# Kernel optimization log

Measured on AMD Instinct MI355X. Metric: run time of the kernel, lower is better.

The kernel has to match this reference:

```python
import jax, jax.numpy as jnp
import numpy as np

NUM_CHUNKS = 8
N = 8192            # points per chunk
STRIDE = 6144
TOTAL = STRIDE * (NUM_CHUNKS - 1) + N  # 51200
OVERLAP_RATIO = 0.3


def setup_inputs() -> dict:
    key = jax.random.key(0)
    ks = jax.random.split(key, 14)
    # Points in a tiny box so all pairwise distances < threshold=0.1 -> full overlap masks.
    chunks = jax.random.uniform(ks[0], (NUM_CHUNKS, N, 3), dtype=jnp.float32) * 0.05
    s = 0.1  # small conv-weight scale keeps smoothed outputs within the threshold box
    return {
        "chunks": chunks,
        "bs_w1": jax.random.normal(ks[1], (32, 3, 5), jnp.float32) * s,
        "bs_b1": jax.random.normal(ks[2], (32,), jnp.float32) * s,
        "bs_w2": jax.random.normal(ks[3], (32, 32, 5), jnp.float32) * s,
        "bs_b2": jax.random.normal(ks[4], (32,), jnp.float32) * s,
        "bs_w3": jax.random.normal(ks[5], (3, 32, 5), jnp.float32) * s,
        "bs_b3": jax.random.normal(ks[6], (3,), jnp.float32) * s,
        "wp_w1": jax.random.normal(ks[7], (32, 6, 1), jnp.float32) * s,
        "wp_b1": jax.random.normal(ks[8], (32,), jnp.float32) * s,
        "wp_w2": jax.random.normal(ks[9], (16, 32, 1), jnp.float32) * s,
        "wp_b2": jax.random.normal(ks[10], (16,), jnp.float32) * s,
        "wp_w3": jax.random.normal(ks[11], (1, 16, 1), jnp.float32) * s,
        "wp_b3": jax.random.normal(ks[12], (1,), jnp.float32) * s,
    }


def _conv1d(x, w, b, pad):
    # x: [Cin, L], w: [Cout, Cin, K] -> [Cout, L]
    y = jax.lax.conv_general_dilated(x[None], w, (1,), [(pad, pad)],
                                     dimension_numbers=("NCH", "OIH", "NCH"))[0]
    return y + b[:, None]


def reference(chunks, bs_w1, bs_b1, bs_w2, bs_b2, bs_w3, bs_b3,
              wp_w1, wp_b1, wp_w2, wp_b2, wp_w3, wp_b3):
    def boundary_smoother(x):   # x: [3, L] -> [3, L]
        h = jax.nn.relu(_conv1d(x, bs_w1, bs_b1, 2))
        h = jax.nn.relu(_conv1d(h, bs_w2, bs_b2, 2))
        return _conv1d(h, bs_w3, bs_b3, 2)

    def weight_predictor(x):    # x: [6, L] -> [L]
        h = jax.nn.relu(_conv1d(x, wp_w1, wp_b1, 0))
        h = jax.nn.relu(_conv1d(h, wp_w2, wp_b2, 0))
        return jax.nn.sigmoid(_conv1d(h, wp_w3, wp_b3, 0))[0]

    def smooth_pair(p, c):      # p, c: [N, 3]; full overlap (masks all-True by construction)
        # squared cdist via the Gram trick; argmin equals cdist argmin
        d2 = (jnp.sum(p * p, 1)[:, None] + jnp.sum(c * c, 1)[None, :]
              - 2.0 * p @ c.T)                       # [N, N]
        mi = jnp.argmin(d2, axis=1)                  # [N]
        matched = c[mi]                              # [N, 3]
        feat = jnp.concatenate([p.T, matched.T], 0)  # [6, N]
        w = weight_predictor(feat)                   # [N]
        fused = w[:, None] * p + (1.0 - w)[:, None] * matched
        sm = boundary_smoother(fused.T).T            # [N, 3]
        # chunk1 fully overlapped -> replaced; chunk2 scatter-written at matched idx
        return sm, c.at[mi].set(sm)

    smoothed = [chunks[0]]
    for i in range(1, NUM_CHUNKS):
        p_new, c_new = smooth_pair(smoothed[-1], chunks[i])
        smoothed[-1] = p_new
        smoothed.append(c_new)
    stacked = jnp.stack(smoothed)                    # [C, N, 3]

    # fade-weighted scatter-add merge
    fade = int(N * OVERLAP_RATIO / 2)
    cw = jnp.ones(N, jnp.float32)
    cw = cw.at[:fade].set(jnp.linspace(0.1, 1.0, fade, dtype=jnp.float32))
    cw = cw.at[-fade:].set(jnp.linspace(1.0, 0.1, fade, dtype=jnp.float32))
    idx = (np.arange(NUM_CHUNKS)[:, None] * STRIDE + np.arange(N)).reshape(-1)
    merged = jnp.zeros((TOTAL, 3), jnp.float32).at[idx].add(
        (stacked * cw[None, :, None]).reshape(-1, 3))
    wsum = jnp.zeros(TOTAL, jnp.float32).at[idx].add(
        jnp.broadcast_to(cw, (NUM_CHUNKS, N)).reshape(-1))
    return merged / jnp.maximum(wsum, 1e-8)[:, None]
```

## Files before the change

### kernel.cpp

```cpp
#include <hip/hip_runtime.h>

#define NPTS 8192
#define NCH 8
#define STRIDE 6144
#define TOTAL 51200
#define FADE 1228
#define SEG 32
#define SEGLEN 256
#define JB 2
#define TEAMS 4
#define TLEN 64
#define SROWS 16

__global__ void k_setup(const float* __restrict__ chunks, float* __restrict__ fin,
                        int* __restrict__ jmax_all, unsigned int* __restrict__ packed32,
                        const float* __restrict__ w2g, float* __restrict__ W2T) {
    int i = blockIdx.x * 256 + threadIdx.x;
    if (i < NCH * NPTS * 3) fin[i] = chunks[i];
    if (i < (NCH - 1) * NPTS) jmax_all[i] = -1;
    if (i < (NCH - 1) * NPTS * 2) packed32[i] = 0xFFFFFFFFu;
    if (i < 5120) {
        int co = i / 160;
        int r = i - co * 160;
        int ci = r / 5;
        int k = r - ci * 5;
        W2T[(ci * 5 + k) * 32 + co] = w2g[i];
    }
}

__global__ __launch_bounds__(1024, 8) void k_argmin(const float* __restrict__ P,
                                                    const float* __restrict__ C,
                                                    unsigned long long* __restrict__ packed) {
#pragma clang fp contract(off)
    __shared__ float4 sh[SEGLEN];
    __shared__ unsigned long long pkbuf[TEAMS - 1][256 * JB];
    int tid = threadIdx.x;
    int lt   = tid & 255;
    int team = tid >> 8;
    int k0 = blockIdx.y * SEGLEN;
    if (tid < SEGLEN) {
        int k = k0 + tid;
        float x = C[k * 3 + 0], y = C[k * 3 + 1], z = C[k * 3 + 2];
        float cc = (x * x + y * y) + z * z;
        sh[tid] = make_float4(x, y, z, cc);
    }
    __syncthreads();
    int j0 = blockIdx.x * (256 * JB) + lt * JB;
    const float2* Pv = (const float2*)(P + j0 * 3);
    float2 a = Pv[0], b = Pv[1], c2 = Pv[2];
    float p0[JB] = {a.x, b.y};
    float p1[JB] = {a.y, c2.x};
    float p2[JB] = {b.x, c2.y};
    float pp[JB], best[JB];
    int bt[JB];
    int t0 = team * TLEN;
#pragma unroll
    for (int i = 0; i < JB; ++i) {
        pp[i] = (p0[i] * p0[i] + p1[i] * p1[i]) + p2[i] * p2[i];
        best[i] = 3.4e38f;
        bt[i] = t0;
    }
#pragma unroll 4
    for (int tt = 0; tt < TLEN; ++tt) {
        int t = t0 + tt;
        float4 f = sh[t];
#pragma unroll
        for (int i = 0; i < JB; ++i) {
            float g = __builtin_fmaf(p2[i], f.z, __builtin_fmaf(p1[i], f.y, p0[i] * f.x));
            float sadd = pp[i] + f.w;
            float d = __builtin_fmaf(-2.0f, g, sadd);
            if (d < best[i]) { best[i] = d; bt[i] = t; }
        }
    }
    unsigned long long pk[JB];
#pragma unroll
    for (int i = 0; i < JB; ++i) {
        unsigned ud = __float_as_uint(best[i]);
        if (ud == 0x80000000u) ud = 0u;
        ud = (ud & 0x80000000u) ? ~ud : (ud | 0x80000000u);
        pk[i] = ((unsigned long long)ud << 32)
              | (unsigned long long)(unsigned)(k0 + bt[i]);
    }
    if (team > 0) {
#pragma unroll
        for (int i = 0; i < JB; ++i) pkbuf[team - 1][lt * JB + i] = pk[i];
    }
    __syncthreads();
    if (team == 0) {
#pragma unroll
        for (int i = 0; i < JB; ++i) {
            unsigned long long v = pk[i];
            unsigned long long v1 = pkbuf[0][lt * JB + i];
            unsigned long long v2 = pkbuf[1][lt * JB + i];
            unsigned long long v3 = pkbuf[2][lt * JB + i];
            if (v1 < v) v = v1;
            if (v2 < v) v = v2;
            if (v3 < v) v = v3;
            atomicMin(&packed[j0 + i], v);
        }
    }
}

__global__ __launch_bounds__(128) void k_resolve(
        const float* __restrict__ P, const float* __restrict__ C,
        const unsigned long long* __restrict__ packed,
        const float* __restrict__ w1g, const float* __restrict__ b1g,
        const float* __restrict__ w2g, const float* __restrict__ b2g,
        const float* __restrict__ w3g, const float* __restrict__ b3g,
        float* __restrict__ fused, int* __restrict__ mi, int* __restrict__ jmax) {
#pragma clang fp contract(off)
    __shared__ float W[780];
    int tid = threadIdx.x;
    for (int i = tid; i < 780; i += 128) {
        float v;
        if (i < 192) v = w1g[i];
        else if (i < 224) v = b1g[i - 192];
        else if (i < 736) v = w2g[i - 224];
        else if (i < 752) v = b2g[i - 736];
        else if (i < 768) v = w3g[i - 752];
        else v = b3g[0];
        W[i] = v;
    }
    __syncthreads();

    int j = blockIdx.x * 128 + tid;
    int m = (int)(unsigned)(packed[j] & 0xFFFFFFFFull);
    mi[j] = m;
    float x6[6];
    x6[0] = P[j * 3 + 0]; x6[1] = P[j * 3 + 1]; x6[2] = P[j * 3 + 2];
    x6[3] = C[m * 3 + 0]; x6[4] = C[m * 3 + 1]; x6[5] = C[m * 3 + 2];

    float h1[32];
#pragma unroll
    for (int o = 0; o < 32; ++o) {
        float acc = 0.0f;
#pragma unroll
        for (int ci = 0; ci < 6; ++ci) acc = __builtin_fmaf(x6[ci], W[o * 6 + ci], acc);
        h1[o] = fmaxf(acc + W[192 + o], 0.0f);
    }
    float h2[16];
#pragma unroll
    for (int o = 0; o < 16; ++o) {
        float acc = 0.0f;
#pragma unroll
        for (int ci = 0; ci < 32; ++ci) acc = __builtin_fmaf(h1[ci], W[224 + o * 32 + ci], acc);
        h2[o] = fmaxf(acc + W[736 + o], 0.0f);
    }
    float acc = 0.0f;
#pragma unroll
    for (int ci = 0; ci < 16; ++ci) acc = __builtin_fmaf(h2[ci], W[752 + ci], acc);
    float z = acc + W[768];
    float w = 1.0f / (1.0f + expf(-z));
    float omw = 1.0f - w;
#pragma unroll
    for (int e = 0; e < 3; ++e) {
        float t1 = w * x6[e];
        float t2 = omw * x6[3 + e];
        fused[e * NPTS + j] = t1 + t2;
    }

    int lane = tid & 63;
    bool issue = true;
    for (int s = 1; s < 64; ++s) {
        int om = __shfl_down(m, s);
        if (lane + s < 64 && om == m) issue = false;
    }
    if (issue) atomicMax(&jmax[m], j);
}

__global__ __launch_bounds__(256) void k_smoother(const float* __restrict__ fused,
        const float* __restrict__ w1g, const float* __restrict__ b1g,
        const float* __restrict__ W2Tg, const float* __restrict__ b2g,
        const float* __restrict__ w3g, const float* __restrict__ b3g,
        float* __restrict__ sm, const int* __restrict__ mi,
        const int* __restrict__ jmax, float* __restrict__ finNext) {
#pragma clang fp contract(off)
    __shared__ float F[3][28];
    __shared__ float H1[32][25];
    __shared__ float H2[32][21];
    __shared__ float W2[5120];
    __shared__ float B2[32];
    int tid = threadIdx.x;
    int BASE = blockIdx.x * SROWS;

    for (int li = tid; li < 84; li += 256) {
        int c = li / 28, i = li % 28;
        int t = BASE - 6 + i;
        F[c][i] = (t >= 0 && t < NPTS) ? fused[c * NPTS + t] : 0.0f;
    }
    for (int li = tid; li < 1280; li += 256)
        ((float4*)W2)[li] = ((const float4*)W2Tg)[li];
    if (tid < 32) B2[tid] = b2g[tid];
    __syncthreads();

    {
        int co = tid >> 3, pg = tid & 7;
        float wr[15];
#pragma unroll
        for (int q = 0; q < 15; ++q) wr[q] = w1g[co * 15 + q];
        float bias = b1g[co];
#pragma unroll
        for (int s = 0; s < 3; ++s) {
            int i = pg * 3 + s;
            int t = BASE - 4 + i;
            float acc = 0.0f;
#pragma unroll
            for (int k = 0; k < 5; ++k)
#pragma unroll
                for (int ci = 0; ci < 3; ++ci)
                    acc = __builtin_fmaf(F[ci][i + k], wr[ci * 5 + k], acc);
            H1[co][i] = (t >= 0 && t < NPTS) ? fmaxf(acc + bias, 0.0f) : 0.0f;
        }
    }
    __syncthreads();

    {
        int cq = tid & 7, pq = tid >> 3;
        if (pq < 10) {
            int i2 = pq * 2;
            int co0 = cq * 4;
            float acc00 = 0.f, acc01 = 0.f, acc02 = 0.f, acc03 = 0.f;
            float acc10 = 0.f, acc11 = 0.f, acc12 = 0.f, acc13 = 0.f;
            for (int k = 0; k < 5; ++k) {
#pragma unroll
                for (int ci = 0; ci < 32; ++ci) {
                    float in0 = H1[ci][i2 + k];
                    float in1 = H1[ci][i2 + k + 1];
                    const float4 wv = *(const float4*)&W2[(ci * 5 + k) * 32 + co0];
                    acc00 = __builtin_fmaf(in0, wv.x, acc00);
                    acc01 = __builtin_fmaf(in0, wv.y, acc01);
                    acc02 = __builtin_fmaf(in0, wv.z, acc02);
                    acc03 = __builtin_fmaf(in0, wv.w, acc03);
                    acc10 = __builtin_fmaf(in1, wv.x, acc10);
                    acc11 = __builtin_fmaf(in1, wv.y, acc11);
                    acc12 = __builtin_fmaf(in1, wv.z, acc12);
                    acc13 = __builtin_fmaf(in1, wv.w, acc13);
                }
            }
            int t0 = BASE - 2 + i2, t1 = t0 + 1;
            bool ok0 = (t0 >= 0 && t0 < NPTS), ok1 = (t1 >= 0 && t1 < NPTS);
            H2[co0 + 0][i2]     = ok0 ? fmaxf(acc00 + B2[co0 + 0], 0.0f) : 0.0f;
            H2[co0 + 1][i2]     = ok0 ? fmaxf(acc01 + B2[co0 + 1], 0.0f) : 0.0f;
            H2[co0 + 2][i2]     = ok0 ? fmaxf(acc02 + B2[co0 + 2], 0.0f) : 0.0f;
            H2[co0 + 3][i2]     = ok0 ? fmaxf(acc03 + B2[co0 + 3], 0.0f) : 0.0f;
            H2[co0 + 0][i2 + 1] = ok1 ? fmaxf(acc10 + B2[co0 + 0], 0.0f) : 0.0f;
            H2[co0 + 1][i2 + 1] = ok1 ? fmaxf(acc11 + B2[co0 + 1], 0.0f) : 0.0f;
            H2[co0 + 2][i2 + 1] = ok1 ? fmaxf(acc12 + B2[co0 + 2], 0.0f) : 0.0f;
            H2[co0 + 3][i2 + 1] = ok1 ? fmaxf(acc13 + B2[co0 + 3], 0.0f) : 0.0f;
        }
    }
    __syncthreads();

    if (tid < 48) {
        int co = tid >> 4, p = tid & 15;
        float wr[160];
        const float4* w3v = (const float4*)(w3g + co * 160);
#pragma unroll
        for (int q = 0; q < 40; ++q) {
            float4 v = w3v[q];
            wr[q * 4 + 0] = v.x; wr[q * 4 + 1] = v.y;
            wr[q * 4 + 2] = v.z; wr[q * 4 + 3] = v.w;
        }
        float acc = 0.0f;
#pragma unroll
        for (int k = 0; k < 5; ++k)
#pragma unroll
            for (int ci = 0; ci < 32; ++ci)
                acc = __builtin_fmaf(H2[ci][p + k], wr[ci * 5 + k], acc);
        float val = acc + b3g[co];
        int jj = BASE + p;
        sm[jj * 3 + co] = val;
        int kk = mi[jj];
        if (jmax[kk] == jj) finNext[kk * 3 + co] = val;
    }
}

__global__ void k_merge(const float* __restrict__ fin, float* __restrict__ out) {
#pragma clang fp contract(off)
    int pos = blockIdx.x * 256 + threadIdx.x;
    if (pos >= TOTAL) return;
    int imax = pos / STRIDE; if (imax > NCH - 1) imax = NCH - 1;
    int imin = (pos >= NPTS) ? ((pos - NPTS) / STRIDE + 1) : 0;
    float a0 = 0.0f, a1 = 0.0f, a2 = 0.0f, wsum = 0.0f;
    const float kstep = 0.9f / 1227.0f;
    for (int i = imin; i <= imax; ++i) {
        int t = pos - i * STRIDE;
        float cw;
        if (t < FADE)                cw = 0.1f + (float)t * kstep;
        else if (t >= NPTS - FADE)   cw = 1.0f - (float)(t - (NPTS - FADE)) * kstep;
        else                         cw = 1.0f;
        const float* v = fin + (i * NPTS + t) * 3;
        a0 += cw * v[0];
        a1 += cw * v[1];
        a2 += cw * v[2];
        wsum += cw;
    }
    float wm = fmaxf(wsum, 1e-8f);
    out[pos * 3 + 0] = a0 / wm;
    out[pos * 3 + 1] = a1 / wm;
    out[pos * 3 + 2] = a2 / wm;
}

extern "C" void kernel_launch(void* const* d_in, const int* in_sizes, int n_in,
                              void* d_out, int out_size, void* d_ws, size_t ws_size,
                              hipStream_t stream) {
    const float* chunks = (const float*)d_in[0];
    const float* bs_w1 = (const float*)d_in[1];
    const float* bs_b1 = (const float*)d_in[2];
    const float* bs_w2 = (const float*)d_in[3];
    const float* bs_b2 = (const float*)d_in[4];
    const float* bs_w3 = (const float*)d_in[5];
    const float* bs_b3 = (const float*)d_in[6];
    const float* wp_w1 = (const float*)d_in[7];
    const float* wp_b1 = (const float*)d_in[8];
    const float* wp_w2 = (const float*)d_in[9];
    const float* wp_b2 = (const float*)d_in[10];
    const float* wp_w3 = (const float*)d_in[11];
    const float* wp_b3 = (const float*)d_in[12];

    unsigned long long* packed_all = (unsigned long long*)d_ws;
    float* fin      = (float*)(packed_all + (NCH - 1) * NPTS);
    float* fused    = fin + NCH * NPTS * 3;
    int*   mi       = (int*)(fused + 3 * NPTS);
    int*   jmax_all = mi + NPTS;
    float* W2T      = (float*)(jmax_all + (NCH - 1) * NPTS);

    k_setup<<<768, 256, 0, stream>>>(chunks, fin, jmax_all, (unsigned int*)packed_all,
                                     bs_w2, W2T);

    for (int i = 1; i < NCH; ++i) {
        const float* C = chunks + i * NPTS * 3;
        float* P  = fin + (i - 1) * NPTS * 3;
        float* Pn = fin + i * NPTS * 3;
        unsigned long long* packed = packed_all + (i - 1) * NPTS;
        int* jmax = jmax_all + (i - 1) * NPTS;

        k_argmin<<<dim3(NPTS / (256 * JB), SEG), 1024, 0, stream>>>(P, C, packed);
        k_resolve<<<64, 128, 0, stream>>>(P, C, packed, wp_w1, wp_b1, wp_w2, wp_b2,
                                          wp_w3, wp_b3, fused, mi, jmax);
        k_smoother<<<NPTS / SROWS, 256, 0, stream>>>(fused, bs_w1, bs_b1, W2T, bs_b2,
                                                     bs_w3, bs_b3, P, mi, jmax, Pn);
    }

    k_merge<<<200, 256, 0, stream>>>(fin, (float*)d_out);
}
```

Measured before the change: 301.1 us.

## Fuse nearest-neighbour argmin with weight predictor into one wave-per-query kernel

Replaces the atomicMin-based split argmin kernel and the separate resolve kernel with one kernel. Each 64-lane wavefront handles one query point, scans all candidates staged through shared memory, and reduces with shuffles. The weight-predictor MLP is then evaluated cooperatively across lanes using shuffles. Candidate points with precomputed squared norms are built once in setup, which removes per-step packed-buffer initialisation, the 64-bit atomics and one launch per step. In exchange each query's scan runs inside a single wave, so a block covers only 16 queries and parallelism per block changes.

```diff
diff --git a/kernel.cpp b/kernel.cpp
--- a/kernel.cpp
+++ b/kernel.cpp
@@ -5,20 +5,26 @@
 #define STRIDE 6144
 #define TOTAL 51200
 #define FADE 1228
-#define SEG 32
-#define SEGLEN 256
-#define JB 2
-#define TEAMS 4
-#define TLEN 64
 #define SROWS 16
+#define QW 16
+
+typedef unsigned long long u64;
 
 __global__ void k_setup(const float* __restrict__ chunks, float* __restrict__ fin,
-                        int* __restrict__ jmax_all, unsigned int* __restrict__ packed32,
+                        int* __restrict__ jmax_all, float4* __restrict__ C4,
                         const float* __restrict__ w2g, float* __restrict__ W2T) {
+#pragma clang fp contract(off)
     int i = blockIdx.x * 256 + threadIdx.x;
     if (i < NCH * NPTS * 3) fin[i] = chunks[i];
-    if (i < (NCH - 1) * NPTS) jmax_all[i] = -1;
-    if (i < (NCH - 1) * NPTS * 2) packed32[i] = 0xFFFFFFFFu;
+    if (i < (NCH - 1) * NPTS) {
+        jmax_all[i] = -1;
+        int c = 1 + (i >> 13);
+        int t = i & (NPTS - 1);
+        const float* s = chunks + ((size_t)c * NPTS + t) * 3;
+        float x = s[0], y = s[1], z = s[2];
+        float cc = (x * x + y * y) + z * z;
+        C4[i] = make_float4(x, y, z, cc);
+    }
     if (i < 5120) {
         int co = i / 160;
         int r = i - co * 160;
@@ -28,144 +34,110 @@
     }
 }
 
-__global__ __launch_bounds__(1024, 8) void k_argmin(const float* __restrict__ P,
-                                                    const float* __restrict__ C,
-                                                    unsigned long long* __restrict__ packed) {
-#pragma clang fp contract(off)
-    __shared__ float4 sh[SEGLEN];
-    __shared__ unsigned long long pkbuf[TEAMS - 1][256 * JB];
-    int tid = threadIdx.x;
-    int lt   = tid & 255;
-    int team = tid >> 8;
-    int k0 = blockIdx.y * SEGLEN;
-    if (tid < SEGLEN) {
-        int k = k0 + tid;
-        float x = C[k * 3 + 0], y = C[k * 3 + 1], z = C[k * 3 + 2];
-        float cc = (x * x + y * y) + z * z;
-        sh[tid] = make_float4(x, y, z, cc);
-    }
-    __syncthreads();
-    int j0 = blockIdx.x * (256 * JB) + lt * JB;
-    const float2* Pv = (const float2*)(P + j0 * 3);
-    float2 a = Pv[0], b = Pv[1], c2 = Pv[2];
-    float p0[JB] = {a.x, b.y};
-    float p1[JB] = {a.y, c2.x};
-    float p2[JB] = {b.x, c2.y};
-    float pp[JB], best[JB];
-    int bt[JB];
-    int t0 = team * TLEN;
-#pragma unroll
-    for (int i = 0; i < JB; ++i) {
-        pp[i] = (p0[i] * p0[i] + p1[i] * p1[i]) + p2[i] * p2[i];
-        best[i] = 3.4e38f;
-        bt[i] = t0;
-    }
-#pragma unroll 4
-    for (int tt = 0; tt < TLEN; ++tt) {
-        int t = t0 + tt;
-        float4 f = sh[t];
-#pragma unroll
-        for (int i = 0; i < JB; ++i) {
-            float g = __builtin_fmaf(p2[i], f.z, __builtin_fmaf(p1[i], f.y, p0[i] * f.x));
-            float sadd = pp[i] + f.w;
-            float d = __builtin_fmaf(-2.0f, g, sadd);
-            if (d < best[i]) { best[i] = d; bt[i] = t; }
-        }
-    }
-    unsigned long long pk[JB];
-#pragma unroll
-    for (int i = 0; i < JB; ++i) {
-        unsigned ud = __float_as_uint(best[i]);
-        if (ud == 0x80000000u) ud = 0u;
-        ud = (ud & 0x80000000u) ? ~ud : (ud | 0x80000000u);
-        pk[i] = ((unsigned long long)ud << 32)
-              | (unsigned long long)(unsigned)(k0 + bt[i]);
-    }
-    if (team > 0) {
-#pragma unroll
-        for (int i = 0; i < JB; ++i) pkbuf[team - 1][lt * JB + i] = pk[i];
-    }
-    __syncthreads();
-    if (team == 0) {
-#pragma unroll
-        for (int i = 0; i < JB; ++i) {
-            unsigned long long v = pk[i];
-            unsigned long long v1 = pkbuf[0][lt * JB + i];
-            unsigned long long v2 = pkbuf[1][lt * JB + i];
-            unsigned long long v3 = pkbuf[2][lt * JB + i];
-            if (v1 < v) v = v1;
-            if (v2 < v) v = v2;
-            if (v3 < v) v = v3;
-            atomicMin(&packed[j0 + i], v);
-        }
-    }
-}
-
-__global__ __launch_bounds__(128) void k_resolve(
-        const float* __restrict__ P, const float* __restrict__ C,
-        const unsigned long long* __restrict__ packed,
-        const float* __restrict__ w1g, const float* __restrict__ b1g,
-        const float* __restrict__ w2g, const float* __restrict__ b2g,
-        const float* __restrict__ w3g, const float* __restrict__ b3g,
+__global__ __launch_bounds__(1024, 8) void k_nn(
+        const float* __restrict__ P, const float4* __restrict__ C4,
+        const float* __restrict__ wp_w1, const float* __restrict__ wp_b1,
+        const float* __restrict__ wp_w2, const float* __restrict__ wp_b2,
+        const float* __restrict__ wp_w3, const float* __restrict__ wp_b3,
         float* __restrict__ fused, int* __restrict__ mi, int* __restrict__ jmax) {
 #pragma clang fp contract(off)
-    __shared__ float W[780];
+    __shared__ float4 sc[1024];
+    __shared__ float Wp[780];
+    __shared__ float Wt2[512];
     int tid = threadIdx.x;
-    for (int i = tid; i < 780; i += 128) {
+    int w = tid >> 6;
+    int lane = tid & 63;
+    int j = blockIdx.x * QW + w;
+
+    if (tid < 780) {
+        int i = tid;
         float v;
-        if (i < 192) v = w1g[i];
-        else if (i < 224) v = b1g[i - 192];
-        else if (i < 736) v = w2g[i - 224];
-        else if (i < 752) v = b2g[i - 736];
-        else if (i < 768) v = w3g[i - 752];
-        else v = b3g[0];
-        W[i] = v;
-    }
-    __syncthreads();
-
-    int j = blockIdx.x * 128 + tid;
-    int m = (int)(unsigned)(packed[j] & 0xFFFFFFFFull);
-    mi[j] = m;
-    float x6[6];
-    x6[0] = P[j * 3 + 0]; x6[1] = P[j * 3 + 1]; x6[2] = P[j * 3 + 2];
-    x6[3] = C[m * 3 + 0]; x6[4] = C[m * 3 + 1]; x6[5] = C[m * 3 + 2];
-
-    float h1[32];
-#pragma unroll
-    for (int o = 0; o < 32; ++o) {
-        float acc = 0.0f;
-#pragma unroll
-        for (int ci = 0; ci < 6; ++ci) acc = __builtin_fmaf(x6[ci], W[o * 6 + ci], acc);
-        h1[o] = fmaxf(acc + W[192 + o], 0.0f);
-    }
-    float h2[16];
-#pragma unroll
-    for (int o = 0; o < 16; ++o) {
-        float acc = 0.0f;
-#pragma unroll
-        for (int ci = 0; ci < 32; ++ci) acc = __builtin_fmaf(h1[ci], W[224 + o * 32 + ci], acc);
-        h2[o] = fmaxf(acc + W[736 + o], 0.0f);
-    }
-    float acc = 0.0f;
-#pragma unroll
-    for (int ci = 0; ci < 16; ++ci) acc = __builtin_fmaf(h2[ci], W[752 + ci], acc);
-    float z = acc + W[768];
-    float w = 1.0f / (1.0f + expf(-z));
-    float omw = 1.0f - w;
-#pragma unroll
-    for (int e = 0; e < 3; ++e) {
-        float t1 = w * x6[e];
-        float t2 = omw * x6[3 + e];
-        fused[e * NPTS + j] = t1 + t2;
-    }
-
-    int lane = tid & 63;
-    bool issue = true;
-    for (int s = 1; s < 64; ++s) {
-        int om = __shfl_down(m, s);
-        if (lane + s < 64 && om == m) issue = false;
-    }
-    if (issue) atomicMax(&jmax[m], j);
+        if (i < 192) v = wp_w1[i];
+        else if (i < 224) v = wp_b1[i - 192];
+        else if (i < 736) v = wp_w2[i - 224];
+        else if (i < 752) v = wp_b2[i - 736];
+        else if (i < 768) v = wp_w3[i - 752];
+        else v = wp_b3[0];
+        Wp[i] = v;
+    }
+    if (tid < 512) {
+        int o = tid >> 5, ci = tid & 31;
+        Wt2[ci * 16 + o] = wp_w2[tid];
+    }
+
+    float p0 = P[j * 3 + 0], p1 = P[j * 3 + 1], p2 = P[j * 3 + 2];
+    float pp = (p0 * p0 + p1 * p1) + p2 * p2;
+    float best = 3.4e38f;
+    int bk = lane;
+
+    float4 pf = C4[tid];
+    for (int s = 0; s < 8; ++s) {
+        __syncthreads();
+        sc[tid] = pf;
+        if (s < 7) pf = C4[(s + 1) * 1024 + tid];
+        __syncthreads();
+        int kbase = s * 1024;
+#pragma unroll
+        for (int u = 0; u < 16; ++u) {
+            float4 f = sc[lane + 64 * u];
+            float g = __builtin_fmaf(p2, f.z, __builtin_fmaf(p1, f.y, p0 * f.x));
+            float sadd = pp + f.w;
+            float d = __builtin_fmaf(-2.0f, g, sadd);
+            int k = kbase + lane + 64 * u;
+            if (d < best) { best = d; bk = k; }
+        }
+    }
+
+    unsigned ud = __float_as_uint(best);
+    if (ud == 0x80000000u) ud = 0u;
+    ud = (ud & 0x80000000u) ? ~ud : (ud | 0x80000000u);
+    unsigned hi = ud;
+    unsigned lo = (unsigned)bk;
+#pragma unroll
+    for (int s = 1; s < 64; s <<= 1) {
+        unsigned ohi = (unsigned)__shfl_xor((int)hi, s);
+        unsigned olo = (unsigned)__shfl_xor((int)lo, s);
+        if (ohi < hi || (ohi == hi && olo < lo)) { hi = ohi; lo = olo; }
+    }
+    int m = (int)lo;
+
+    float4 cm = C4[m];
+    int c1 = lane & 31;
+    float acc1 = 0.0f;
+    acc1 = __builtin_fmaf(p0,   Wp[c1 * 6 + 0], acc1);
+    acc1 = __builtin_fmaf(p1,   Wp[c1 * 6 + 1], acc1);
+    acc1 = __builtin_fmaf(p2,   Wp[c1 * 6 + 2], acc1);
+    acc1 = __builtin_fmaf(cm.x, Wp[c1 * 6 + 3], acc1);
+    acc1 = __builtin_fmaf(cm.y, Wp[c1 * 6 + 4], acc1);
+    acc1 = __builtin_fmaf(cm.z, Wp[c1 * 6 + 5], acc1);
+    float h1 = fmaxf(acc1 + Wp[192 + c1], 0.0f);
+
+    int c2 = lane & 15;
+    float acc2 = 0.0f;
+#pragma unroll
+    for (int ci = 0; ci < 32; ++ci)
+        acc2 = __builtin_fmaf(__shfl(h1, ci), Wt2[ci * 16 + c2], acc2);
+    float h2 = fmaxf(acc2 + Wp[736 + c2], 0.0f);
+
+    float acc3 = 0.0f;
+#pragma unroll
+    for (int ci = 0; ci < 16; ++ci)
+        acc3 = __builtin_fmaf(__shfl(h2, ci), Wp[752 + ci], acc3);
+    float z = acc3 + Wp[768];
+    float ww = 1.0f / (1.0f + expf(-z));
+    float omw = 1.0f - ww;
+
+    if (lane < 3) {
+        float xe = (lane == 0) ? p0 : (lane == 1) ? p1 : p2;
+        float ce = (lane == 0) ? cm.x : (lane == 1) ? cm.y : cm.z;
+        float t1 = ww * xe;
+        float t2 = omw * ce;
+        fused[lane * NPTS + j] = t1 + t2;
+    }
+    if (lane == 0) {
+        mi[j] = m;
+        atomicMax(&jmax[m], j);
+    }
 }
 
 __global__ __launch_bounds__(256) void k_smoother(const float* __restrict__ fused,
@@ -318,26 +290,23 @@
     const float* wp_w3 = (const float*)d_in[11];
     const float* wp_b3 = (const float*)d_in[12];
 
-    unsigned long long* packed_all = (unsigned long long*)d_ws;
-    float* fin      = (float*)(packed_all + (NCH - 1) * NPTS);
+    float4* C4all   = (float4*)d_ws;
+    float* fin      = (float*)(C4all + (NCH - 1) * NPTS);
     float* fused    = fin + NCH * NPTS * 3;
     int*   mi       = (int*)(fused + 3 * NPTS);
     int*   jmax_all = mi + NPTS;
     float* W2T      = (float*)(jmax_all + (NCH - 1) * NPTS);
 
-    k_setup<<<768, 256, 0, stream>>>(chunks, fin, jmax_all, (unsigned int*)packed_all,
-                                     bs_w2, W2T);
+    k_setup<<<768, 256, 0, stream>>>(chunks, fin, jmax_all, C4all, bs_w2, W2T);
 
     for (int i = 1; i < NCH; ++i) {
-        const float* C = chunks + i * NPTS * 3;
         float* P  = fin + (i - 1) * NPTS * 3;
         float* Pn = fin + i * NPTS * 3;
-        unsigned long long* packed = packed_all + (i - 1) * NPTS;
+        const float4* C4 = C4all + (size_t)(i - 1) * NPTS;
         int* jmax = jmax_all + (i - 1) * NPTS;
 
-        k_argmin<<<dim3(NPTS / (256 * JB), SEG), 1024, 0, stream>>>(P, C, packed);
-        k_resolve<<<64, 128, 0, stream>>>(P, C, packed, wp_w1, wp_b1, wp_w2, wp_b2,
-                                          wp_w3, wp_b3, fused, mi, jmax);
+        k_nn<<<NPTS / QW, 1024, 0, stream>>>(P, C4, wp_w1, wp_b1, wp_w2, wp_b2,
+                                             wp_w3, wp_b3, fused, mi, jmax);
         k_smoother<<<NPTS / SROWS, 256, 0, stream>>>(fused, bs_w1, bs_b1, W2T, bs_b2,
                                                      bs_w3, bs_b3, P, mi, jmax, Pn);
     }
```

Result: slower. 390.2 us (+29.6%).
